# Kernel optimization log

Measured on AMD Instinct MI355X. Metric: run time of the kernel, lower is better.

Reference implementation:

```python
import jax, jax.numpy as jnp
import numpy as np
from jax import lax

B, S, T = 2048, 4096, 3


def setup_inputs() -> dict:
    key = jax.random.key(0)
    k_em, k_tr, k_st, k_en, k_tg = jax.random.split(key, 5)
    emissions = jax.random.normal(k_em, (B, S, T), dtype=jnp.float32)
    # reset_parameters(): uniform(-0.1, 0.1)
    transitions = jax.random.uniform(k_tr, (T, T), minval=-0.1, maxval=0.1, dtype=jnp.float32)
    start_transitions = jax.random.uniform(k_st, (T,), minval=-0.1, maxval=0.1, dtype=jnp.float32)
    end_transitions = jax.random.uniform(k_en, (T,), minval=-0.1, maxval=0.1, dtype=jnp.float32)
    tags = jax.random.randint(k_tg, (B, S), 0, T, dtype=jnp.int32)
    mask = jnp.ones((B, S), dtype=jnp.int32)
    return {
        "emissions": emissions,
        "transitions": transitions,
        "start_transitions": start_transitions,
        "end_transitions": end_transitions,
        "tags": tags,
        "mask": mask,
    }


def _crf_nll(emissions, transitions, start_transitions, end_transitions, tags, mask):
    # batch_first=True -> transpose to time-major (S, B, ...)
    em = jnp.transpose(emissions, (1, 0, 2))  # (S, B, T)
    tg = jnp.transpose(tags, (1, 0))          # (S, B)
    mk = jnp.transpose(mask, (1, 0))          # (S, B)
    batch_idx = jnp.arange(em.shape[1])

    # ---- log partition (forward algorithm) ----
    alpha0 = start_transitions[None, :] + em[0]  # (B, T)

    def fwd_step(alpha, inp):
        e, m = inp  # e: (B,T), m: (B,)
        # alpha[b,i] + trans[i,j] + e[b,j] -> logsumexp over i
        nxt = jax.nn.logsumexp(alpha[:, :, None] + transitions[None, :, :] + e[:, None, :], axis=1)
        alpha = jnp.where((m > 0)[:, None], nxt, alpha)
        return alpha, None

    alpha, _ = lax.scan(fwd_step, alpha0, (em[1:], mk[1:]))
    log_partition = jax.nn.logsumexp(alpha + end_transitions[None, :], axis=1)  # (B,)

    # ---- gold score ----
    score0 = start_transitions[tg[0]] + em[0][batch_idx, tg[0]]  # (B,)

    def score_step(carry, inp):
        score, prev = carry
        e, t, m = inp
        add = transitions[prev, t] + e[batch_idx, t]
        score = score + jnp.where(m > 0, add, jnp.zeros_like(score))
        return (score, t), None

    (score, _), _ = lax.scan(score_step, (score0, tg[0]), (em[1:], tg[1:], mk[1:]))
    seq_lens = jnp.sum(mk, axis=0)  # (B,)
    last_tags = tg[seq_lens - 1, batch_idx]
    score = score + end_transitions[last_tags]

    return jnp.mean(log_partition - score)


def reference(emissions, transitions, start_transitions, end_transitions, tags, mask):
    return _crf_nll(emissions, transitions, start_transitions, end_transitions, tags, mask)
```

## Files before the change

### kernel.cpp

```cpp
#include <hip/hip_runtime.h>
#include <math.h>

#define CRF_B 2048
#define CRF_S 4096
#define LN2F  0.6931471805599453f

#define CRF_MERGE(aq0,aq1,aq2,aq3,aq4,aq5,aq6,aq7,aq8,aC,asc,acn, \
                  bq0,bq1,bq2,bq3,bq4,bq5,bq6,bq7,bq8,bC,bsc,bcn) { \
    float r0_=aq0*bq0+aq1*bq3+aq2*bq6;                              \
    float r1_=aq0*bq1+aq1*bq4+aq2*bq7;                              \
    float r2_=aq0*bq2+aq1*bq5+aq2*bq8;                              \
    float r3_=aq3*bq0+aq4*bq3+aq5*bq6;                              \
    float r4_=aq3*bq1+aq4*bq4+aq5*bq7;                              \
    float r5_=aq3*bq2+aq4*bq5+aq5*bq8;                              \
    float r6_=aq6*bq0+aq7*bq3+aq8*bq6;                              \
    float r7_=aq6*bq1+aq7*bq4+aq8*bq7;                              \
    float r8_=aq6*bq2+aq7*bq5+aq8*bq8;                              \
    float mx_ = fmaxf(fmaxf(fmaxf(fmaxf(r0_,r1_),r2_),              \
                            fmaxf(fmaxf(r3_,r4_),r5_)),             \
                      fmaxf(fmaxf(r6_,r7_),r8_));                   \
    int ex_ = ((__float_as_int(mx_)>>23)&255)-127;                  \
    float sc_ = __int_as_float((127-ex_)<<23);                      \
    aq0=r0_*sc_; aq1=r1_*sc_; aq2=r2_*sc_;                          \
    aq3=r3_*sc_; aq4=r4_*sc_; aq5=r5_*sc_;                          \
    aq6=r6_*sc_; aq7=r7_*sc_; aq8=r8_*sc_;                          \
    aC = aC + bC + ex_;                                             \
    asc += bsc; acn += bcn; }

#define CRF_STEP(tconst, E0, E1, E2) {                               \
    int tv_ = (int)((ttag >> (2*(tconst))) & 3u);                    \
    int mv_ = (int)((tmsk >> (tconst)) & 1u);                        \
    if (mv_ && !(((tconst) == 0) && (tid == 0))) {                   \
        float X0_ = __expf(E0), X1_ = __expf(E1), X2_ = __expf(E2);  \
        float n0_, n1_, n2_;                                         \
        n0_ = q0*Etr0 + q1*Etr3 + q2*Etr6;                           \
        n1_ = q0*Etr1 + q1*Etr4 + q2*Etr7;                           \
        n2_ = q0*Etr2 + q1*Etr5 + q2*Etr8;                           \
        q0 = n0_*X0_; q1 = n1_*X1_; q2 = n2_*X2_;                    \
        n0_ = q3*Etr0 + q4*Etr3 + q5*Etr6;                           \
        n1_ = q3*Etr1 + q4*Etr4 + q5*Etr7;                           \
        n2_ = q3*Etr2 + q4*Etr5 + q5*Etr8;                           \
        q3 = n0_*X0_; q4 = n1_*X1_; q5 = n2_*X2_;                    \
        n0_ = q6*Etr0 + q7*Etr3 + q8*Etr6;                           \
        n1_ = q6*Etr1 + q7*Etr4 + q8*Etr7;                           \
        n2_ = q6*Etr2 + q7*Etr5 + q8*Etr8;                           \
        q6 = n0_*X0_; q7 = n1_*X1_; q8 = n2_*X2_;                    \
        sem += (tv_ == 0) ? (E0) : ((tv_ == 1) ? (E1) : (E2));       \
    } }

#define CRF_RENORM() {                                               \
    float mx_ = fmaxf(fmaxf(fmaxf(fmaxf(q0,q1),q2),                  \
                            fmaxf(fmaxf(q3,q4),q5)),                 \
                      fmaxf(fmaxf(q6,q7),q8));                       \
    int ex_ = ((__float_as_int(mx_) >> 23) & 255) - 127;             \
    float sc_ = __int_as_float((127 - ex_) << 23);                   \
    q0 *= sc_; q1 *= sc_; q2 *= sc_;                                 \
    q3 *= sc_; q4 *= sc_; q5 *= sc_;                                 \
    q6 *= sc_; q7 *= sc_; q8 *= sc_;                                 \
    C += ex_; }

__global__ __launch_bounds__(256, 5) void crf_row_kernel(
    const float* __restrict__ em,
    const float* __restrict__ trans,
    const float* __restrict__ startt,
    const float* __restrict__ endt,
    const int*   __restrict__ tags,
    const int*   __restrict__ mask,
    float* __restrict__ perb)
{
    __shared__ float s_tr[9];
    __shared__ float s_rq[4][10];
    __shared__ int   s_rc[4][2];

    const int tid = threadIdx.x;
    const int w = tid >> 6, l = tid & 63;
    const int b = blockIdx.x;
    const long cbase = (long)b * CRF_S + (long)tid * 16;

    if (tid < 9) s_tr[tid] = trans[tid];
    __syncthreads();

    const int4* t4 = (const int4*)(tags + cbase);
    const int4* m4 = (const int4*)(mask + cbase);
    int4 ta = t4[0], tb = t4[1], tc = t4[2], td = t4[3];
    int4 ma = m4[0], mb = m4[1], mc = m4[2], md = m4[3];
    int p = 0;
    if (tid > 0) p = tags[cbase - 1];

    unsigned ttag =  (unsigned)(ta.x & 3)        | ((unsigned)(ta.y & 3) << 2)
                  | ((unsigned)(ta.z & 3) << 4)  | ((unsigned)(ta.w & 3) << 6)
                  | ((unsigned)(tb.x & 3) << 8)  | ((unsigned)(tb.y & 3) << 10)
                  | ((unsigned)(tb.z & 3) << 12) | ((unsigned)(tb.w & 3) << 14)
                  | ((unsigned)(tc.x & 3) << 16) | ((unsigned)(tc.y & 3) << 18)
                  | ((unsigned)(tc.z & 3) << 20) | ((unsigned)(tc.w & 3) << 22)
                  | ((unsigned)(td.x & 3) << 24) | ((unsigned)(td.y & 3) << 26)
                  | ((unsigned)(td.z & 3) << 28) | ((unsigned)(td.w & 3) << 30);
    unsigned tmsk =  (unsigned)(ma.x != 0)        | ((unsigned)(ma.y != 0) << 1)
                  | ((unsigned)(ma.z != 0) << 2)  | ((unsigned)(ma.w != 0) << 3)
                  | ((unsigned)(mb.x != 0) << 4)  | ((unsigned)(mb.y != 0) << 5)
                  | ((unsigned)(mb.z != 0) << 6)  | ((unsigned)(mb.w != 0) << 7)
                  | ((unsigned)(mc.x != 0) << 8)  | ((unsigned)(mc.y != 0) << 9)
                  | ((unsigned)(mc.z != 0) << 10) | ((unsigned)(mc.w != 0) << 11)
                  | ((unsigned)(md.x != 0) << 12) | ((unsigned)(md.y != 0) << 13)
                  | ((unsigned)(md.z != 0) << 14) | ((unsigned)(md.w != 0) << 15);

    float str_sum = 0.f;
    {
        int pr = p;
        #pragma unroll
        for (int t = 0; t < 16; ++t) {
            int tv = (int)((ttag >> (2 * t)) & 3u);
            if (((tmsk >> t) & 1u) && !((t == 0) && (tid == 0)))
                str_sum += s_tr[pr * 3 + tv];
            pr = tv;
        }
    }
    int cnt = __popc(tmsk & ((tid == 0) ? 0xFFFEu : 0xFFFFu));

    float Etr0 = __expf(s_tr[0]), Etr1 = __expf(s_tr[1]), Etr2 = __expf(s_tr[2]);
    float Etr3 = __expf(s_tr[3]), Etr4 = __expf(s_tr[4]), Etr5 = __expf(s_tr[5]);
    float Etr6 = __expf(s_tr[6]), Etr7 = __expf(s_tr[7]), Etr8 = __expf(s_tr[8]);

    float q0=1.f,q1=0.f,q2=0.f, q3=0.f,q4=1.f,q5=0.f, q6=0.f,q7=0.f,q8=1.f;
    int C = 0;
    float sem = 0.f;

    const float4* e4 = (const float4*)(em + cbase * 3);
    float4 c0 = e4[0], c1 = e4[1], c2 = e4[2];
    float et0 = c0.x, et1 = c0.y, et2 = c0.z;

    #pragma unroll
    for (int g = 0; g < 4; ++g) {
        float4 f0, f1, f2;
        if (g < 3) { f0 = e4[3*g+3]; f1 = e4[3*g+4]; f2 = e4[3*g+5]; }
        CRF_STEP(4*g + 0, c0.x, c0.y, c0.z);
        CRF_STEP(4*g + 1, c0.w, c1.x, c1.y);
        CRF_STEP(4*g + 2, c1.z, c1.w, c2.x);
        CRF_STEP(4*g + 3, c2.y, c2.z, c2.w);
        CRF_RENORM();
        c0 = f0; c1 = f1; c2 = f2;
    }
    float score = str_sum + sem;

    #pragma unroll
    for (int st = 1; st < 64; st <<= 1) {
        float nq0 = __shfl_down(q0, st), nq1 = __shfl_down(q1, st),
              nq2 = __shfl_down(q2, st), nq3 = __shfl_down(q3, st),
              nq4 = __shfl_down(q4, st), nq5 = __shfl_down(q5, st),
              nq6 = __shfl_down(q6, st), nq7 = __shfl_down(q7, st),
              nq8 = __shfl_down(q8, st);
        int   nC  = __shfl_down(C, st);
        float nsc = __shfl_down(score, st);
        int   ncn = __shfl_down(cnt, st);
        CRF_MERGE(q0,q1,q2,q3,q4,q5,q6,q7,q8,C,score,cnt,
                  nq0,nq1,nq2,nq3,nq4,nq5,nq6,nq7,nq8,nC,nsc,ncn);
    }

    if (l == 0) {
        s_rq[w][0]=q0; s_rq[w][1]=q1; s_rq[w][2]=q2;
        s_rq[w][3]=q3; s_rq[w][4]=q4; s_rq[w][5]=q5;
        s_rq[w][6]=q6; s_rq[w][7]=q7; s_rq[w][8]=q8;
        s_rq[w][9]=score;
        s_rc[w][0]=C;  s_rc[w][1]=cnt;
    }
    __syncthreads();

    if (tid == 0) {
        float a0=q0, a1=q1, a2=q2, a3=q3, a4=q4, a5=q5, a6=q6, a7=q7, a8=q8;
        float asc = score;
        int AC = C, acn = cnt;
        #pragma unroll
        for (int w2 = 1; w2 < 4; ++w2) {
            float m0=s_rq[w2][0], m1=s_rq[w2][1], m2=s_rq[w2][2],
                  m3=s_rq[w2][3], m4=s_rq[w2][4], m5=s_rq[w2][5],
                  m6=s_rq[w2][6], m7=s_rq[w2][7], m8=s_rq[w2][8];
            float msc = s_rq[w2][9];
            int mC = s_rc[w2][0], mcn = s_rc[w2][1];
            CRF_MERGE(a0,a1,a2,a3,a4,a5,a6,a7,a8,AC,asc,acn,
                      m0,m1,m2,m3,m4,m5,m6,m7,m8,mC,msc,mcn);
        }
        int tg0 = (int)(ttag & 3u), mk0 = (int)(tmsk & 1u);
        float la0 = startt[0] + et0;
        float la1 = startt[1] + et1;
        float la2 = startt[2] + et2;
        float am = fmaxf(fmaxf(la0, la1), la2);
        float w0  = __expf(la0 - am);
        float w1  = __expf(la1 - am);
        float w2v = __expf(la2 - am);
        float v0 = w0*a0 + w1*a3 + w2v*a6;
        float v1 = w0*a1 + w1*a4 + w2v*a7;
        float v2 = w0*a2 + w1*a5 + w2v*a8;
        float sum = v0 * __expf(endt[0]) + v1 * __expf(endt[1])
                  + v2 * __expf(endt[2]);
        float lp = am + (float)AC * LN2F + __logf(sum);

        float sc = asc + startt[tg0]
                 + ((tg0 == 0) ? et0 : (tg0 == 1) ? et1 : et2);
        int cn = acn + mk0;
        int lastidx = (cn > 0) ? (cn - 1) : 0;
        sc += endt[tags[(long)b * CRF_S + lastidx]];

        perb[b] = lp - sc;
    }
}

__global__ __launch_bounds__(256) void crf_reduce_kernel(
    const float* __restrict__ perb, float* __restrict__ out)
{
    __shared__ float sdata[256];
    const int tid = threadIdx.x;
    float s = 0.f;
    for (int i = tid; i < CRF_B; i += 256) s += perb[i];
    sdata[tid] = s;
    __syncthreads();
    for (int off = 128; off > 0; off >>= 1) {
        if (tid < off) sdata[tid] += sdata[tid + off];
        __syncthreads();
    }
    if (tid == 0) out[0] = sdata[0] * (1.0f / (float)CRF_B);
}

extern "C" void kernel_launch(void* const* d_in, const int* in_sizes, int n_in,
                              void* d_out, int out_size, void* d_ws, size_t ws_size,
                              hipStream_t stream)
{
    const float* em     = (const float*)d_in[0];
    const float* trans  = (const float*)d_in[1];
    const float* startt = (const float*)d_in[2];
    const float* endt   = (const float*)d_in[3];
    const int*   tags   = (const int*)d_in[4];
    const int*   mask   = (const int*)d_in[5];
    float* out = (float*)d_out;

    float* perb = (float*)d_ws;

    crf_row_kernel<<<CRF_B, 256, 0, stream>>>(
        em, trans, startt, endt, tags, mask, perb);
    crf_reduce_kernel<<<1, 256, 0, stream>>>(perb, out);
}
```

Baseline: 40.40 us.

## Stage emissions through LDS as fp16 with coalesced loads and packed tags

Each wave now loads its 1024-timestep slice of emissions with fully coalesced float4 reads, converts them to half precision and writes them into a padded shared-memory tile. Tags and masks are read coalesced as well and packed into 16-bit words. Each thread then reads back its own 16 timesteps from LDS. This replaces the strided per-thread global loads, but it adds about 29 KB of LDS per block, which may limit occupancy. Rounding emissions to fp16 also adds precision error to both the partition function and the gold score.

```diff
diff --git a/kernel.cpp b/kernel.cpp
--- a/kernel.cpp
+++ b/kernel.cpp
@@ -1,9 +1,13 @@
 #include <hip/hip_runtime.h>
+#include <hip/hip_fp16.h>
 #include <math.h>
 
 #define CRF_B 2048
 #define CRF_S 4096
 #define LN2F  0.6931471805599453f
+
+#define ULO(u) __low2float(*(const __half2*)&(u))
+#define UHI(u) __high2float(*(const __half2*)&(u))
 
 #define CRF_MERGE(aq0,aq1,aq2,aq3,aq4,aq5,aq6,aq7,aq8,aC,asc,acn, \
                   bq0,bq1,bq2,bq3,bq4,bq5,bq6,bq7,bq8,bC,bsc,bcn) { \
@@ -31,7 +35,8 @@
     int tv_ = (int)((ttag >> (2*(tconst))) & 3u);                    \
     int mv_ = (int)((tmsk >> (tconst)) & 1u);                        \
     if (mv_ && !(((tconst) == 0) && (tid == 0))) {                   \
-        float X0_ = __expf(E0), X1_ = __expf(E1), X2_ = __expf(E2);  \
+        float e0_ = (E0), e1_ = (E1), e2_ = (E2);                    \
+        float X0_ = __expf(e0_), X1_ = __expf(e1_), X2_ = __expf(e2_); \
         float n0_, n1_, n2_;                                         \
         n0_ = q0*Etr0 + q1*Etr3 + q2*Etr6;                           \
         n1_ = q0*Etr1 + q1*Etr4 + q2*Etr7;                           \
@@ -45,7 +50,7 @@
         n1_ = q6*Etr1 + q7*Etr4 + q8*Etr7;                           \
         n2_ = q6*Etr2 + q7*Etr5 + q8*Etr8;                           \
         q6 = n0_*X0_; q7 = n1_*X1_; q8 = n2_*X2_;                    \
-        sem += (tv_ == 0) ? (E0) : ((tv_ == 1) ? (E1) : (E2));       \
+        sem += (tv_ == 0) ? e0_ : ((tv_ == 1) ? e1_ : e2_);          \
     } }
 
 #define CRF_RENORM() {                                               \
@@ -68,6 +73,8 @@
     const int*   __restrict__ mask,
     float* __restrict__ perb)
 {
+    __shared__ __half         s_em[4][64 * 56];
+    __shared__ unsigned short s_tm[4][256];
     __shared__ float s_tr[9];
     __shared__ float s_rq[4][10];
     __shared__ int   s_rc[4][2];
@@ -76,33 +83,59 @@
     const int w = tid >> 6, l = tid & 63;
     const int b = blockIdx.x;
     const long cbase = (long)b * CRF_S + (long)tid * 16;
+    const long wbase = (long)b * CRF_S + (long)w * 1024;
 
     if (tid < 9) s_tr[tid] = trans[tid];
+
+    const float4* gsrc = (const float4*)(em + wbase * 3);
+    __half* emw = &s_em[w][0];
+    #pragma unroll
+    for (int k = 0; k < 12; ++k) {
+        int g = k * 64 + l;
+        float4 v = gsrc[g];
+        int c = (g * 683) >> 13;
+        int r = (g - c * 12) * 4;
+        __half2 ha = __floats2half2_rn(v.x, v.y);
+        __half2 hb = __floats2half2_rn(v.z, v.w);
+        uint2 pk;
+        pk.x = *(unsigned*)&ha; pk.y = *(unsigned*)&hb;
+        *(uint2*)(emw + c * 56 + r) = pk;
+    }
+    const int4* t4 = (const int4*)(tags + wbase);
+    const int4* m4 = (const int4*)(mask + wbase);
+    #pragma unroll
+    for (int k = 0; k < 4; ++k) {
+        int g = k * 64 + l;
+        int4 tg = t4[g];
+        int4 mk = m4[g];
+        unsigned u = (unsigned)(tg.x & 3)        | ((unsigned)(tg.y & 3) << 2)
+                   | ((unsigned)(tg.z & 3) << 4) | ((unsigned)(tg.w & 3) << 6)
+                   | ((unsigned)(mk.x != 0) << 8) | ((unsigned)(mk.y != 0) << 9)
+                   | ((unsigned)(mk.z != 0) << 10)| ((unsigned)(mk.w != 0) << 11);
+        s_tm[w][g] = (unsigned short)u;
+    }
+    int p = 0;
+    if (tid > 0) p = tags[cbase - 1] & 3;
+
     __syncthreads();
 
-    const int4* t4 = (const int4*)(tags + cbase);
-    const int4* m4 = (const int4*)(mask + cbase);
-    int4 ta = t4[0], tb = t4[1], tc = t4[2], td = t4[3];
-    int4 ma = m4[0], mb = m4[1], mc = m4[2], md = m4[3];
-    int p = 0;
-    if (tid > 0) p = tags[cbase - 1];
-
-    unsigned ttag =  (unsigned)(ta.x & 3)        | ((unsigned)(ta.y & 3) << 2)
-                  | ((unsigned)(ta.z & 3) << 4)  | ((unsigned)(ta.w & 3) << 6)
-                  | ((unsigned)(tb.x & 3) << 8)  | ((unsigned)(tb.y & 3) << 10)
-                  | ((unsigned)(tb.z & 3) << 12) | ((unsigned)(tb.w & 3) << 14)
-                  | ((unsigned)(tc.x & 3) << 16) | ((unsigned)(tc.y & 3) << 18)
-                  | ((unsigned)(tc.z & 3) << 20) | ((unsigned)(tc.w & 3) << 22)
-                  | ((unsigned)(td.x & 3) << 24) | ((unsigned)(td.y & 3) << 26)
-                  | ((unsigned)(td.z & 3) << 28) | ((unsigned)(td.w & 3) << 30);
-    unsigned tmsk =  (unsigned)(ma.x != 0)        | ((unsigned)(ma.y != 0) << 1)
-                  | ((unsigned)(ma.z != 0) << 2)  | ((unsigned)(ma.w != 0) << 3)
-                  | ((unsigned)(mb.x != 0) << 4)  | ((unsigned)(mb.y != 0) << 5)
-                  | ((unsigned)(mb.z != 0) << 6)  | ((unsigned)(mb.w != 0) << 7)
-                  | ((unsigned)(mc.x != 0) << 8)  | ((unsigned)(mc.y != 0) << 9)
-                  | ((unsigned)(mc.z != 0) << 10) | ((unsigned)(mc.w != 0) << 11)
-                  | ((unsigned)(md.x != 0) << 12) | ((unsigned)(md.y != 0) << 13)
-                  | ((unsigned)(md.z != 0) << 14) | ((unsigned)(md.w != 0) << 15);
+    const char* cbytes = (const char*)(emw) + 112 * l;
+    uint4 ua = *(const uint4*)(cbytes +  0);
+    uint4 ub = *(const uint4*)(cbytes + 16);
+    uint4 uc = *(const uint4*)(cbytes + 32);
+    uint4 ud = *(const uint4*)(cbytes + 48);
+    uint4 ue = *(const uint4*)(cbytes + 64);
+    uint4 uf = *(const uint4*)(cbytes + 80);
+    ushort4 tmv = *(const ushort4*)&s_tm[w][4 * l];
+
+    unsigned ttag =  (unsigned)(tmv.x & 0xff)
+                  | ((unsigned)(tmv.y & 0xff) << 8)
+                  | ((unsigned)(tmv.z & 0xff) << 16)
+                  | ((unsigned)(tmv.w & 0xff) << 24);
+    unsigned tmsk =  (unsigned)((tmv.x >> 8) & 0xf)
+                  | ((unsigned)((tmv.y >> 8) & 0xf) << 4)
+                  | ((unsigned)((tmv.z >> 8) & 0xf) << 8)
+                  | ((unsigned)((tmv.w >> 8) & 0xf) << 12);
 
     float str_sum = 0.f;
     {
@@ -125,21 +158,29 @@
     int C = 0;
     float sem = 0.f;
 
-    const float4* e4 = (const float4*)(em + cbase * 3);
-    float4 c0 = e4[0], c1 = e4[1], c2 = e4[2];
-    float et0 = c0.x, et1 = c0.y, et2 = c0.z;
-
-    #pragma unroll
-    for (int g = 0; g < 4; ++g) {
-        float4 f0, f1, f2;
-        if (g < 3) { f0 = e4[3*g+3]; f1 = e4[3*g+4]; f2 = e4[3*g+5]; }
-        CRF_STEP(4*g + 0, c0.x, c0.y, c0.z);
-        CRF_STEP(4*g + 1, c0.w, c1.x, c1.y);
-        CRF_STEP(4*g + 2, c1.z, c1.w, c2.x);
-        CRF_STEP(4*g + 3, c2.y, c2.z, c2.w);
-        CRF_RENORM();
-        c0 = f0; c1 = f1; c2 = f2;
-    }
+    float et0 = ULO(ua.x), et1 = UHI(ua.x), et2 = ULO(ua.y);
+
+    CRF_STEP( 0, ULO(ua.x), UHI(ua.x), ULO(ua.y));
+    CRF_STEP( 1, UHI(ua.y), ULO(ua.z), UHI(ua.z));
+    CRF_STEP( 2, ULO(ua.w), UHI(ua.w), ULO(ub.x));
+    CRF_STEP( 3, UHI(ub.x), ULO(ub.y), UHI(ub.y));
+    CRF_RENORM();
+    CRF_STEP( 4, ULO(ub.z), UHI(ub.z), ULO(ub.w));
+    CRF_STEP( 5, UHI(ub.w), ULO(uc.x), UHI(uc.x));
+    CRF_STEP( 6, ULO(uc.y), UHI(uc.y), ULO(uc.z));
+    CRF_STEP( 7, UHI(uc.z), ULO(uc.w), UHI(uc.w));
+    CRF_RENORM();
+    CRF_STEP( 8, ULO(ud.x), UHI(ud.x), ULO(ud.y));
+    CRF_STEP( 9, UHI(ud.y), ULO(ud.z), UHI(ud.z));
+    CRF_STEP(10, ULO(ud.w), UHI(ud.w), ULO(ue.x));
+    CRF_STEP(11, UHI(ue.x), ULO(ue.y), UHI(ue.y));
+    CRF_RENORM();
+    CRF_STEP(12, ULO(ue.z), UHI(ue.z), ULO(ue.w));
+    CRF_STEP(13, UHI(ue.w), ULO(uf.x), UHI(uf.x));
+    CRF_STEP(14, ULO(uf.y), UHI(uf.y), ULO(uf.z));
+    CRF_STEP(15, UHI(uf.z), ULO(uf.w), UHI(uf.w));
+    CRF_RENORM();
+
     float score = str_sum + sem;
 
     #pragma unroll
```

Result: slower. 41.95 us (+3.8%).
